# Optimization experiments

Hardware: AMD Instinct MI355X
Metric: run time of the kernel (lower is better)

## Reference

```python
import jax, jax.numpy as jnp
import numpy as np

N = 50000      # nodes
E = 1600000    # edges (before self loops)
F = 128        # input_dim
H = 4          # num_heads
D = 32         # hidden_dim (per head)
B = 16         # graphs in batch
NEG_SLOPE = 0.2  # PyG GATv2Conv default negative_slope


def setup_inputs() -> dict:
    key = jax.random.key(0)
    ks = jax.random.split(key, 8)
    x = jax.random.normal(ks[0], (N, F), dtype=jnp.float32)
    edge_index = jax.random.randint(ks[1], (2, E), 0, N, dtype=jnp.int32)
    batch = jnp.sort(jax.random.randint(ks[2], (N,), 0, B, dtype=jnp.int32))
    s = 0.05
    W_l = jax.random.normal(ks[3], (F, H * D), dtype=jnp.float32) * s
    b_l = jnp.zeros((H * D,), dtype=jnp.float32)
    W_r = jax.random.normal(ks[4], (F, H * D), dtype=jnp.float32) * s
    b_r = jnp.zeros((H * D,), dtype=jnp.float32)
    att = jax.random.normal(ks[5], (H, D), dtype=jnp.float32) * s
    bias = jnp.zeros((H * D,), dtype=jnp.float32)
    return {"x": x, "edge_index": edge_index, "batch": batch,
            "W_l": W_l, "b_l": b_l, "W_r": W_r, "b_r": b_r,
            "att": att, "bias": bias}


def reference(x, edge_index, batch, W_l, b_l, W_r, b_r, att, bias):
    n = x.shape[0]
    # PyG GATv2Conv adds self loops by default
    loops = jnp.arange(n, dtype=edge_index.dtype)
    src = jnp.concatenate([edge_index[0], loops])  # message source j
    dst = jnp.concatenate([edge_index[1], loops])  # message target i

    xl = (x @ W_l + b_l).reshape(n, H, D)  # source transform
    xr = (x @ W_r + b_r).reshape(n, H, D)  # target transform

    # per-edge GATv2 attention logits: a^T LeakyReLU(xl_j + xr_i)
    m = xl[src] + xr[dst]                                   # [E+N, H, D]
    e = jnp.sum(jax.nn.leaky_relu(m, NEG_SLOPE) * att, -1)  # [E+N, H]

    # softmax over incoming edges of each destination node
    e_max = jax.ops.segment_max(e, dst, num_segments=n)
    ex = jnp.exp(e - e_max[dst])
    den = jax.ops.segment_sum(ex, dst, num_segments=n)
    alpha = ex / den[dst]                                   # [E+N, H]

    # weighted scatter-sum aggregation of source features
    out = jax.ops.segment_sum(alpha[..., None] * xl[src], dst, num_segments=n)
    out = out.reshape(n, H * D) + bias                      # concat heads + bias
    out = jax.nn.relu(out)

    # global max pool over nodes of each graph
    pooled = jax.ops.segment_max(out, batch, num_segments=B)
    pooled = jnp.where(jnp.isfinite(pooled), pooled, 0.0)   # guard empty graphs
    return pooled
```

## Files before the change

### kernel.cpp

```cpp
#include <hip/hip_runtime.h>

#define NN 50000
#define NE 1600000
#define FDIM 128
#define CDIM 128
#define NGRAPH 16
#define SLOPE 0.2f
#define CSTRIDE 96
#define BINSH 7
#define NBIN 391
#define EPB 6400
#define NB1 250
#define EPT 25
#define CAP 5120
#define POOL_NODES 64
#define POOL_NB ((NN + POOL_NODES - 1) / POOL_NODES)
#define TNB 782

__device__ __forceinline__ unsigned short f2bf(float f) {
    unsigned u = __float_as_uint(f);
    return (unsigned short)((u + 0x7FFFu + ((u >> 16) & 1u)) >> 16);
}
__device__ __forceinline__ unsigned packbf(float a, float b) {
    return (unsigned)f2bf(a) | ((unsigned)f2bf(b) << 16);
}
__device__ __forceinline__ unsigned short f2h(float f) {
    union { _Float16 h; unsigned short u; } c;
    c.h = (_Float16)f;
    return c.u;
}

typedef __attribute__((ext_vector_type(8))) short short8;
typedef __attribute__((ext_vector_type(4))) float f32x4;
typedef _Float16 h2 __attribute__((ext_vector_type(2)));
union FragU { uint4 u; short8 s; };
union HU    { uint4 u; h2 h[4]; };

__device__ __forceinline__ float qadd_xor1(float d) {
#if __has_builtin(__builtin_amdgcn_update_dpp)
    int x = __builtin_amdgcn_update_dpp(0, __float_as_int(d), 0xB1, 0xF, 0xF, true);
    return d + __int_as_float(x);
#else
    return d + __shfl_xor(d, 1);
#endif
}
__device__ __forceinline__ float qadd_xor2(float d) {
#if __has_builtin(__builtin_amdgcn_update_dpp)
    int x = __builtin_amdgcn_update_dpp(0, __float_as_int(d), 0x4E, 0xF, 0xF, true);
    return d + __int_as_float(x);
#else
    return d + __shfl_xor(d, 2);
#endif
}

__global__ __launch_bounds__(256) void k_init(
    float* __restrict__ out, int* __restrict__ gbin_cnt,
    const float* __restrict__ Wl, const float* __restrict__ Wr,
    uint4* __restrict__ wpack) {
    const int b = blockIdx.x;
    if (b < 16) {
        int C = b * 256 + threadIdx.x;
        const float* W = (C < 2048) ? Wl : Wr;
        int c = C & 2047;
        int ccol = c & 15, cq = (c >> 4) & 3, ckq = (c >> 6) & 3, cnt_ = c >> 8;
        const float* wp = &W[(size_t)(ckq * 32 + cq * 8) * CDIM + cnt_ * 16 + ccol];
        uint4 u;
        u.x = packbf(wp[0],        wp[CDIM]);
        u.y = packbf(wp[2*CDIM],   wp[3*CDIM]);
        u.z = packbf(wp[4*CDIM],   wp[5*CDIM]);
        u.w = packbf(wp[6*CDIM],   wp[7*CDIM]);
        wpack[C] = u;
    } else {
        int i = (b - 16) * 256 + threadIdx.x;
        if (i < NGRAPH * CDIM) out[i] = 0.f;
        if (i < NBIN) gbin_cnt[i] = 0;
    }
}

__global__ __launch_bounds__(256) void k_front(
    const float* __restrict__ x,
    const float* __restrict__ bl, const float* __restrict__ br,
    const int* __restrict__ src, const int* __restrict__ dst,
    int* __restrict__ gbin_cnt, unsigned* __restrict__ gstage,
    unsigned short* __restrict__ xlh, unsigned short* __restrict__ xrh,
    const uint4* __restrict__ wpack) {
    __shared__ __align__(16) char shraw[32768];
    const int tid = threadIdx.x;

    if (blockIdx.x < NB1) {
        int* bcnt = (int*)shraw;
        int* boff = bcnt + NBIN;
        int* gb   = boff + NBIN;
        int* sc   = gb + NBIN;
        unsigned* st = (unsigned*)(sc + 256);
        const int t  = tid;
        const int e0 = blockIdx.x * EPB;

        for (int b = t; b < NBIN; b += 256) bcnt[b] = 0;
        __syncthreads();

        unsigned sd[EPT]; int bn[EPT]; int pl[EPT];
#pragma unroll
        for (int k = 0; k < EPT; k++) {
            int e = e0 + k * 256 + t;
            int s = src[e], d = dst[e];
            bn[k] = d >> BINSH;
            sd[k] = (unsigned)s | ((unsigned)(d & 127) << 16)
                                | ((unsigned)bn[k] << 23);
            pl[k] = atomicAdd(&bcnt[bn[k]], 1);
        }
        __syncthreads();

        int c0 = (2*t     < NBIN) ? bcnt[2*t]     : 0;
        int c1 = (2*t + 1 < NBIN) ? bcnt[2*t + 1] : 0;
        int v  = c0 + c1;
        sc[t] = v; __syncthreads();
        for (int off = 1; off < 256; off <<= 1) {
            int add = (t >= off) ? sc[t - off] : 0;
            __syncthreads();
            sc[t] += add;
            __syncthreads();
        }
        int base = sc[t] - v;
        if (2*t     < NBIN) boff[2*t]     = base;
        if (2*t + 1 < NBIN) boff[2*t + 1] = base + c0;
        __syncthreads();

        for (int b = t; b < NBIN; b += 256) {
            int c = bcnt[b];
            gb[b] = (c > 0) ? atomicAdd(&gbin_cnt[b], c) : 0;
        }
#pragma unroll
        for (int k = 0; k < EPT; k++) st[boff[bn[k]] + pl[k]] = sd[k];
        __syncthreads();

        for (int idx = t; idx < EPB; idx += 256) {
            unsigned w = st[idx];
            int b = w >> 23;
            int p = gb[b] + (idx - boff[b]);
            if (p < CAP) gstage[(size_t)b * CAP + p] = w;
        }
    } else {
        uint4* wfrag = (uint4*)shraw;
        const int bid   = blockIdx.x - NB1;
        const int wv    = tid >> 6;
        const int lane  = tid & 63;
        const int quad  = lane >> 4;
        const int col   = lane & 15;
        const int node0 = bid * 64;
        const int nodeA = node0 + wv * 16 + col;
        const bool aval = nodeA < NN;

        FragU afrag[4];
#pragma unroll
        for (int kq = 0; kq < 4; kq++) {
            float4 lo = make_float4(0.f,0.f,0.f,0.f), hi = lo;
            if (aval) {
                const float* ap = &x[(size_t)nodeA * FDIM + kq * 32 + quad * 8];
                lo = *(const float4*)ap;
                hi = *(const float4*)(ap + 4);
            }
            afrag[kq].u.x = packbf(lo.x, lo.y);
            afrag[kq].u.y = packbf(lo.z, lo.w);
            afrag[kq].u.z = packbf(hi.x, hi.y);
            afrag[kq].u.w = packbf(hi.z, hi.w);
        }

        const int myrow0 = node0 + wv * 16 + quad * 4;

        for (int mat = 0; mat < 2; mat++) {
            const float* bb = mat ? br : bl;
            unsigned short* dsto = mat ? xrh : xlh;
            const uint4* wsrc = wpack + mat * 2048;
            __syncthreads();
#pragma unroll
            for (int i = 0; i < 8; i++)
                wfrag[i * 256 + tid] = wsrc[i * 256 + tid];
            __syncthreads();

#pragma unroll
            for (int nt = 0; nt < 8; nt++) {
                f32x4 acc = {0.f, 0.f, 0.f, 0.f};
#pragma unroll
                for (int kq = 0; kq < 4; kq++) {
                    FragU bfr;
                    bfr.u = wfrag[(nt * 4 + kq) * 64 + lane];
                    acc = __builtin_amdgcn_mfma_f32_16x16x32_bf16(
                              afrag[kq].s, bfr.s, acc, 0, 0, 0);
                }
                int ch = nt * 16 + col;
                float bv = bb[ch];
#pragma unroll
                for (int r = 0; r < 4; r++) {
                    int node = myrow0 + r;
                    if (node < NN)
                        dsto[(size_t)node * CDIM + ch] = f2h(acc[r] + bv);
                }
            }
        }
    }
}

__global__ __launch_bounds__(512) void k_csr(
    const int* __restrict__ gbin_cnt, const unsigned* __restrict__ gstage,
    int* __restrict__ cnt, unsigned short* __restrict__ colp) {
    __shared__ int nfill[128];
    __shared__ unsigned short crow[128 * CSTRIDE];
    const int bin = blockIdx.x;
    const int t   = threadIdx.x;
    const int n0  = bin << BINSH;
    const int nb  = min(128, NN - n0);
    const int m   = min(gbin_cnt[bin], CAP);

    if (t < 128) nfill[t] = 0;
    __syncthreads();

    unsigned w[10];
    bool     ok[10];
#pragma unroll
    for (int k = 0; k < 10; k++) {
        int i = k * 512 + t;
        ok[k] = i < m;
        if (ok[k]) w[k] = gstage[(size_t)bin * CAP + i];
    }
#pragma unroll
    for (int k = 0; k < 10; k++) {
        if (ok[k]) {
            int dl = (w[k] >> 16) & 127;
            int p  = atomicAdd(&nfill[dl], 1);
            if (p < CSTRIDE - 1)
                crow[dl * CSTRIDE + p] = (unsigned short)(w[k] & 0xFFFF);
        }
    }
    __syncthreads();

    if (t < nb) {
        int c = min(nfill[t], CSTRIDE - 1);
        crow[t * CSTRIDE + c] = (unsigned short)(n0 + t);
        cnt[n0 + t] = c + 1;
    }
    __syncthreads();

    unsigned* gout = (unsigned*)colp + (size_t)bin * (128 * CSTRIDE / 2);
    const unsigned* cin = (const unsigned*)crow;
    for (int idx = t; idx < 128 * CSTRIDE / 2; idx += 512) gout[idx] = cin[idx];
}

__device__ __forceinline__ void edge_compute(
    uint4 qu,
    const h2* __restrict__ rx, const h2* __restrict__ ah,
    float& s, float* __restrict__ acc) {
    HU q; q.u = qu;
    const h2 c02 = {(_Float16)SLOPE, (_Float16)SLOPE};
    float d = 0.f;
#pragma unroll
    for (int k = 0; k < 4; k++) {
        h2 t  = q.h[k] + rx[k];
        h2 lk = __builtin_elementwise_max(t, t * c02);
#if __has_builtin(__builtin_amdgcn_fdot2)
        d = __builtin_amdgcn_fdot2(lk, ah[k], d, false);
#else
        d = fmaf((float)lk.x, (float)ah[k].x, d);
        d = fmaf((float)lk.y, (float)ah[k].y, d);
#endif
    }
    d = qadd_xor1(d);
    d = qadd_xor2(d);
    float w = __expf(d);
    s += w;
#pragma unroll
    for (int k = 0; k < 4; k++) {
        acc[2*k]   = fmaf(w, (float)q.h[k].x, acc[2*k]);
        acc[2*k+1] = fmaf(w, (float)q.h[k].y, acc[2*k+1]);
    }
}

__device__ __forceinline__ void edge_body(
    const char* __restrict__ xlb, unsigned chb, int j,
    const h2* __restrict__ rx, const h2* __restrict__ ah,
    float& s, float* __restrict__ acc) {
    uint4 qu = *(const uint4*)(xlb + (((unsigned)j << 8) | chb));
    edge_compute(qu, rx, ah, s, acc);
}

__global__ __launch_bounds__(256) void k_aggregate(
    const unsigned short* __restrict__ xlh, const unsigned short* __restrict__ xrh,
    const float* __restrict__ att, const float* __restrict__ bias,
    const int* __restrict__ cnt, const unsigned short* __restrict__ colp,
    float* __restrict__ nodeout) {
    const int wave = blockIdx.x * 4 + (threadIdx.x >> 6);
    const int lane = threadIdx.x & 63;
    const int i     = wave;
    const size_t start = (size_t)i * CSTRIDE;
    const int deg   = cnt[i];
    const int grp   = lane >> 4;
    const int ch0   = (lane & 15) * 8;
    const unsigned chb = (unsigned)(ch0 * 2);
    const char* xlb = (const char*)xlh;

    int cj0 = (int)colp[start + lane];
    int cj1 = 0;
    if (deg > 64) cj1 = (int)colp[start + 64 + lane];

    HU rxu;
    rxu.u = *(const uint4*)&xrh[(size_t)i * CDIM + ch0];
    const float4 aa0 = *(const float4*)&att[ch0];
    const float4 aa1 = *(const float4*)&att[ch0 + 4];
    h2 ah[4];
    ah[0] = h2{(_Float16)aa0.x, (_Float16)aa0.y};
    ah[1] = h2{(_Float16)aa0.z, (_Float16)aa0.w};
    ah[2] = h2{(_Float16)aa1.x, (_Float16)aa1.y};
    ah[3] = h2{(_Float16)aa1.z, (_Float16)aa1.w};

    float s = 0.f;
    float acc[8];
#pragma unroll
    for (int k = 0; k < 8; k++) acc[k] = 0.f;

    const int full = deg >> 2;
    const int f0   = full < 16 ? full : 16;

    if (f0 > 0) {
        int ja = __shfl(cj0, grp);
        uint4 qa = *(const uint4*)(xlb + (((unsigned)ja << 8) | chb));
        if (f0 > 1) {
            int jb = __shfl(cj0, 4 + grp);
            uint4 qb = *(const uint4*)(xlb + (((unsigned)jb << 8) | chb));
            for (int t = 0; t + 2 < f0; t++) {
                int jc = __shfl(cj0, (t + 2) * 4 + grp);
                uint4 qc = *(const uint4*)(xlb + (((unsigned)jc << 8) | chb));
                edge_compute(qa, rxu.h, ah, s, acc);
                qa = qb; qb = qc;
            }
            edge_compute(qa, rxu.h, ah, s, acc);
            edge_compute(qb, rxu.h, ah, s, acc);
        } else {
            edge_compute(qa, rxu.h, ah, s, acc);
        }
    }
    for (int t = 16; t < full; t++) {
        int j = __shfl(cj1, t * 4 + grp - 64);
        edge_body(xlb, chb, j, rxu.h, ah, s, acc);
    }
    int e  = full * 4 + grp;
    int jt = (e < 64) ? __shfl(cj0, e) : __shfl(cj1, (e - 64) & 63);
    if (e < deg)
        edge_body(xlb, chb, jt, rxu.h, ah, s, acc);

#pragma unroll
    for (int dist = 16; dist <= 32; dist <<= 1) {
        s += __shfl_xor(s, dist);
#pragma unroll
        for (int k = 0; k < 8; k++) acc[k] += __shfl_xor(acc[k], dist);
    }

    if (grp == 0) {
        float inv = 1.f / s;
        float4 o0, o1;
        const float4 b0 = *(const float4*)&bias[ch0];
        const float4 b1 = *(const float4*)&bias[ch0 + 4];
        o0.x = fmaxf(fmaf(acc[0], inv, b0.x), 0.f);
        o0.y = fmaxf(fmaf(acc[1], inv, b0.y), 0.f);
        o0.z = fmaxf(fmaf(acc[2], inv, b0.z), 0.f);
        o0.w = fmaxf(fmaf(acc[3], inv, b0.w), 0.f);
        o1.x = fmaxf(fmaf(acc[4], inv, b1.x), 0.f);
        o1.y = fmaxf(fmaf(acc[5], inv, b1.y), 0.f);
        o1.z = fmaxf(fmaf(acc[6], inv, b1.z), 0.f);
        o1.w = fmaxf(fmaf(acc[7], inv, b1.w), 0.f);
        float* op = &nodeout[(size_t)i * CDIM + ch0];
        *(float4*)op       = o0;
        *(float4*)(op + 4) = o1;
    }
}

__global__ __launch_bounds__(256) void k_pool(
    const float* __restrict__ nodeout, const int* __restrict__ batch,
    float* __restrict__ out) {
    const int tid  = threadIdx.x;
    const int c4   = (tid & 31) * 4;
    const int nl   = tid >> 5;
    const int base = blockIdx.x * POOL_NODES;
    float4 mx = make_float4(0.f, 0.f, 0.f, 0.f);
    int cur = -1;
#pragma unroll
    for (int k = 0; k < POOL_NODES / 8; k++) {
        int node = base + k * 8 + nl;
        if (node >= NN) break;
        int g = batch[node];
        if (g != cur) {
            if (cur >= 0) {
                int* op = (int*)&out[cur * CDIM + c4];
                if (mx.x > 0.f) atomicMax(op,     __float_as_int(mx.x));
                if (mx.y > 0.f) atomicMax(op + 1, __float_as_int(mx.y));
                if (mx.z > 0.f) atomicMax(op + 2, __float_as_int(mx.z));
                if (mx.w > 0.f) atomicMax(op + 3, __float_as_int(mx.w));
            }
            cur = g;
            mx = make_float4(0.f, 0.f, 0.f, 0.f);
        }
        float4 v = *(const float4*)&nodeout[(size_t)node * CDIM + c4];
        mx.x = fmaxf(mx.x, v.x);
        mx.y = fmaxf(mx.y, v.y);
        mx.z = fmaxf(mx.z, v.z);
        mx.w = fmaxf(mx.w, v.w);
    }
    if (cur >= 0) {
        int* op = (int*)&out[cur * CDIM + c4];
        if (mx.x > 0.f) atomicMax(op,     __float_as_int(mx.x));
        if (mx.y > 0.f) atomicMax(op + 1, __float_as_int(mx.y));
        if (mx.z > 0.f) atomicMax(op + 2, __float_as_int(mx.z));
        if (mx.w > 0.f) atomicMax(op + 3, __float_as_int(mx.w));
    }
}

extern "C" void kernel_launch(void* const* d_in, const int* in_sizes, int n_in,
                              void* d_out, int out_size, void* d_ws, size_t ws_size,
                              hipStream_t stream) {
    const float* x     = (const float*)d_in[0];
    const int*   ei    = (const int*)d_in[1];
    const int*   batch = (const int*)d_in[2];
    const float* Wl    = (const float*)d_in[3];
    const float* bl    = (const float*)d_in[4];
    const float* Wr    = (const float*)d_in[5];
    const float* br    = (const float*)d_in[6];
    const float* att   = (const float*)d_in[7];
    const float* bias  = (const float*)d_in[8];
    float* out = (float*)d_out;

    char* w = (char*)d_ws;
    float*          nodeout  = (float*)w;          w += (size_t)NN * CDIM * 4;
    unsigned short* xlh      = (unsigned short*)w; w += (size_t)NN * CDIM * 2;
    unsigned short* xrh      = (unsigned short*)w; w += (size_t)NN * CDIM * 2;
    int*            cnt      = (int*)w;            w += (size_t)NN * 4;
    unsigned short* colp     = (unsigned short*)w; w += (size_t)NBIN * 128 * CSTRIDE * 2;
    unsigned*       gstage   = (unsigned*)w;       w += (size_t)NBIN * CAP * 4;
    int*            gbin_cnt = (int*)w;            w += (size_t)NBIN * 4;
    uint4*          wpack    = (uint4*)w;          w += (size_t)4096 * 16;

    const int* src = ei;
    const int* dst = ei + NE;

    k_init<<<26, 256, 0, stream>>>(out, gbin_cnt, Wl, Wr, wpack);
    k_front<<<NB1 + TNB, 256, 0, stream>>>(x, bl, br,
                                           src, dst, gbin_cnt, gstage, xlh, xrh,
                                           wpack);
    k_csr<<<NBIN, 512, 0, stream>>>(gbin_cnt, gstage, cnt, colp);
    k_aggregate<<<NN / 4, 256, 0, stream>>>(xlh, xrh, att, bias,
                                            cnt, colp, nodeout);
    k_pool<<<POOL_NB, 256, 0, stream>>>(nodeout, batch, out);
}
```

Before: 225.7 us.

## Use fp16 accumulation, exp2 softmax, batched edge loads, and direct weight reads

The aggregation kernel now accumulates weighted source features in packed fp16 instead of fp32. It folds log2(e) into the attention vector so the exponential becomes a native exp2, and it issues all of the first 16 edge-group gathers up front into registers instead of a rolling two-deep prefetch. The projection path stops staging packed weights through shared memory with barriers and reads the fragments straight from global memory. This cuts ALU work and register traffic and exposes more memory parallelism, at the cost of higher register pressure and fp16 accumulation error in the unnormalized sums.

```diff
diff --git a/kernel.cpp b/kernel.cpp
--- a/kernel.cpp
+++ b/kernel.cpp
@@ -16,6 +16,7 @@
 #define POOL_NODES 64
 #define POOL_NB ((NN + POOL_NODES - 1) / POOL_NODES)
 #define TNB 782
+#define LOG2E 1.4426950408889634f
 
 __device__ __forceinline__ unsigned short f2bf(float f) {
     unsigned u = __float_as_uint(f);
@@ -35,6 +36,7 @@
 typedef _Float16 h2 __attribute__((ext_vector_type(2)));
 union FragU { uint4 u; short8 s; };
 union HU    { uint4 u; h2 h[4]; };
+union HI    { h2 h; int i; };
 
 __device__ __forceinline__ float qadd_xor1(float d) {
 #if __has_builtin(__builtin_amdgcn_update_dpp)
@@ -50,6 +52,13 @@
     return d + __int_as_float(x);
 #else
     return d + __shfl_xor(d, 2);
+#endif
+}
+__device__ __forceinline__ float exp2fast(float d) {
+#if __has_builtin(__builtin_amdgcn_exp2f)
+    return __builtin_amdgcn_exp2f(d);
+#else
+    return __expf(d * 0.6931471805599453f);
 #endif
 }
 
@@ -141,7 +150,6 @@
             if (p < CAP) gstage[(size_t)b * CAP + p] = w;
         }
     } else {
-        uint4* wfrag = (uint4*)shraw;
         const int bid   = blockIdx.x - NB1;
         const int wv    = tid >> 6;
         const int lane  = tid & 63;
@@ -168,15 +176,11 @@
 
         const int myrow0 = node0 + wv * 16 + quad * 4;
 
+#pragma unroll
         for (int mat = 0; mat < 2; mat++) {
             const float* bb = mat ? br : bl;
             unsigned short* dsto = mat ? xrh : xlh;
             const uint4* wsrc = wpack + mat * 2048;
-            __syncthreads();
-#pragma unroll
-            for (int i = 0; i < 8; i++)
-                wfrag[i * 256 + tid] = wsrc[i * 256 + tid];
-            __syncthreads();
 
 #pragma unroll
             for (int nt = 0; nt < 8; nt++) {
@@ -184,7 +188,7 @@
 #pragma unroll
                 for (int kq = 0; kq < 4; kq++) {
                     FragU bfr;
-                    bfr.u = wfrag[(nt * 4 + kq) * 64 + lane];
+                    bfr.u = wsrc[(nt * 4 + kq) * 64 + lane];
                     acc = __builtin_amdgcn_mfma_f32_16x16x32_bf16(
                               afrag[kq].s, bfr.s, acc, 0, 0, 0);
                 }
@@ -249,7 +253,7 @@
 __device__ __forceinline__ void edge_compute(
     uint4 qu,
     const h2* __restrict__ rx, const h2* __restrict__ ah,
-    float& s, float* __restrict__ acc) {
+    float& s, h2* __restrict__ acch) {
     HU q; q.u = qu;
     const h2 c02 = {(_Float16)SLOPE, (_Float16)SLOPE};
     float d = 0.f;
@@ -266,21 +270,21 @@
     }
     d = qadd_xor1(d);
     d = qadd_xor2(d);
-    float w = __expf(d);
+    float w = exp2fast(d);
     s += w;
-#pragma unroll
-    for (int k = 0; k < 4; k++) {
-        acc[2*k]   = fmaf(w, (float)q.h[k].x, acc[2*k]);
-        acc[2*k+1] = fmaf(w, (float)q.h[k].y, acc[2*k+1]);
-    }
+    _Float16 wh = (_Float16)w;
+    h2 w2 = {wh, wh};
+#pragma unroll
+    for (int k = 0; k < 4; k++)
+        acch[k] += w2 * q.h[k];
 }
 
 __device__ __forceinline__ void edge_body(
     const char* __restrict__ xlb, unsigned chb, int j,
     const h2* __restrict__ rx, const h2* __restrict__ ah,
-    float& s, float* __restrict__ acc) {
+    float& s, h2* __restrict__ acch) {
     uint4 qu = *(const uint4*)(xlb + (((unsigned)j << 8) | chb));
-    edge_compute(qu, rx, ah, s, acc);
+    edge_compute(qu, rx, ah, s, acch);
 }
 
 __global__ __launch_bounds__(256) void k_aggregate(
@@ -307,51 +311,52 @@
     const float4 aa0 = *(const float4*)&att[ch0];
     const float4 aa1 = *(const float4*)&att[ch0 + 4];
     h2 ah[4];
-    ah[0] = h2{(_Float16)aa0.x, (_Float16)aa0.y};
-    ah[1] = h2{(_Float16)aa0.z, (_Float16)aa0.w};
-    ah[2] = h2{(_Float16)aa1.x, (_Float16)aa1.y};
-    ah[3] = h2{(_Float16)aa1.z, (_Float16)aa1.w};
+    ah[0] = h2{(_Float16)(aa0.x*LOG2E), (_Float16)(aa0.y*LOG2E)};
+    ah[1] = h2{(_Float16)(aa0.z*LOG2E), (_Float16)(aa0.w*LOG2E)};
+    ah[2] = h2{(_Float16)(aa1.x*LOG2E), (_Float16)(aa1.y*LOG2E)};
+    ah[3] = h2{(_Float16)(aa1.z*LOG2E), (_Float16)(aa1.w*LOG2E)};
 
     float s = 0.f;
-    float acc[8];
-#pragma unroll
-    for (int k = 0; k < 8; k++) acc[k] = 0.f;
+    h2 acch[4];
+#pragma unroll
+    for (int k = 0; k < 4; k++) acch[k] = h2{(_Float16)0.f, (_Float16)0.f};
 
     const int full = deg >> 2;
     const int f0   = full < 16 ? full : 16;
 
-    if (f0 > 0) {
-        int ja = __shfl(cj0, grp);
-        uint4 qa = *(const uint4*)(xlb + (((unsigned)ja << 8) | chb));
-        if (f0 > 1) {
-            int jb = __shfl(cj0, 4 + grp);
-            uint4 qb = *(const uint4*)(xlb + (((unsigned)jb << 8) | chb));
-            for (int t = 0; t + 2 < f0; t++) {
-                int jc = __shfl(cj0, (t + 2) * 4 + grp);
-                uint4 qc = *(const uint4*)(xlb + (((unsigned)jc << 8) | chb));
-                edge_compute(qa, rxu.h, ah, s, acc);
-                qa = qb; qb = qc;
-            }
-            edge_compute(qa, rxu.h, ah, s, acc);
-            edge_compute(qb, rxu.h, ah, s, acc);
-        } else {
-            edge_compute(qa, rxu.h, ah, s, acc);
-        }
-    }
+    uint4 q[16];
+#pragma unroll
+    for (int k = 0; k < 16; k++) {
+        if (k < f0) {
+            int j = __shfl(cj0, k * 4 + grp);
+            q[k] = *(const uint4*)(xlb + (((unsigned)j << 8) | chb));
+        }
+    }
+#pragma unroll
+    for (int k = 0; k < 16; k++) {
+        if (k < f0)
+            edge_compute(q[k], rxu.h, ah, s, acch);
+    }
+
     for (int t = 16; t < full; t++) {
         int j = __shfl(cj1, t * 4 + grp - 64);
-        edge_body(xlb, chb, j, rxu.h, ah, s, acc);
+        edge_body(xlb, chb, j, rxu.h, ah, s, acch);
     }
     int e  = full * 4 + grp;
     int jt = (e < 64) ? __shfl(cj0, e) : __shfl(cj1, (e - 64) & 63);
     if (e < deg)
-        edge_body(xlb, chb, jt, rxu.h, ah, s, acc);
+        edge_body(xlb, chb, jt, rxu.h, ah, s, acch);
 
 #pragma unroll
     for (int dist = 16; dist <= 32; dist <<= 1) {
         s += __shfl_xor(s, dist);
 #pragma unroll
-        for (int k = 0; k < 8; k++) acc[k] += __shfl_xor(acc[k], dist);
+        for (int k = 0; k < 4; k++) {
+            HI a, b;
+            a.h = acch[k];
+            b.i = __shfl_xor(a.i, dist);
+            acch[k] = a.h + b.h;
+        }
     }
 
     if (grp == 0) {
@@ -359,14 +364,14 @@
         float4 o0, o1;
         const float4 b0 = *(const float4*)&bias[ch0];
         const float4 b1 = *(const float4*)&bias[ch0 + 4];
-        o0.x = fmaxf(fmaf(acc[0], inv, b0.x), 0.f);
-        o0.y = fmaxf(fmaf(acc[1], inv, b0.y), 0.f);
-        o0.z = fmaxf(fmaf(acc[2], inv, b0.z), 0.f);
-        o0.w = fmaxf(fmaf(acc[3], inv, b0.w), 0.f);
-        o1.x = fmaxf(fmaf(acc[4], inv, b1.x), 0.f);
-        o1.y = fmaxf(fmaf(acc[5], inv, b1.y), 0.f);
-        o1.z = fmaxf(fmaf(acc[6], inv, b1.z), 0.f);
-        o1.w = fmaxf(fmaf(acc[7], inv, b1.w), 0.f);
+        o0.x = fmaxf(fmaf((float)acch[0].x, inv, b0.x), 0.f);
+        o0.y = fmaxf(fmaf((float)acch[0].y, inv, b0.y), 0.f);
+        o0.z = fmaxf(fmaf((float)acch[1].x, inv, b0.z), 0.f);
+        o0.w = fmaxf(fmaf((float)acch[1].y, inv, b0.w), 0.f);
+        o1.x = fmaxf(fmaf((float)acch[2].x, inv, b1.x), 0.f);
+        o1.y = fmaxf(fmaf((float)acch[2].y, inv, b1.y), 0.f);
+        o1.z = fmaxf(fmaf((float)acch[3].x, inv, b1.z), 0.f);
+        o1.w = fmaxf(fmaf((float)acch[3].y, inv, b1.w), 0.f);
         float* op = &nodeout[(size_t)i * CDIM + ch0];
         *(float4*)op       = o0;
         *(float4*)(op + 4) = o1;
```

New measurement: 231.7 us. 2.6% more time.
